# Kernel optimization log

Hardware: AMD Instinct MI355X
Metric: run time of the kernel (lower is better)

The kernel has to match this reference:

```python
import jax, jax.numpy as jnp
import numpy as np
from functools import partial

HID = 320
RF = 4
EPS = 1e-5


def lstm_scan(x_seq, Wih, Whh, bih, bhh):
    """PyTorch-style single-layer LSTM. x_seq: [T,B,D] -> outputs [T,B,H]."""
    T, B, _ = x_seq.shape
    H = Whh.shape[1]
    b = bih + bhh  # [4H]
    # precompute input projections for all steps: [T,B,4H]
    xg = jnp.einsum('tbd,gd->tbg', x_seq, Wih) + b

    def step(carry, xg_t):
        h, c = carry
        gates = xg_t + h @ Whh.T  # [B,4H]
        i, f, g, o = jnp.split(gates, 4, axis=-1)  # torch gate order i,f,g,o
        i = jax.nn.sigmoid(i)
        f = jax.nn.sigmoid(f)
        g = jnp.tanh(g)
        o = jax.nn.sigmoid(o)
        c = f * c + i * g
        h = o * jnp.tanh(c)
        return (h, c), h

    h0 = jnp.zeros((B, H), x_seq.dtype)
    (_, _), ys = jax.lax.scan(step, (h0, h0), xg)
    return ys


def conv2d(x, w, b):
    y = jax.lax.conv_general_dilated(x, w, (1, 1), 'VALID',
                                     dimension_numbers=('NCHW', 'OIHW', 'NCHW'))
    return y + b[None, :, None, None]


def maxpool2(x):
    return jax.lax.reduce_window(x, -jnp.inf, jax.lax.max,
                                 (1, 1, 2, 2), (1, 1, 2, 2), 'VALID')


def batchnorm(x, g, b):
    # training-mode BN (batch statistics, biased variance) like nn.BatchNorm2d
    m = x.mean((0, 2, 3), keepdims=True)
    v = x.var((0, 2, 3), keepdims=True)
    return (x - m) * jax.lax.rsqrt(v + EPS) * g[None, :, None, None] + b[None, :, None, None]


def setup_inputs() -> dict:
    key = jax.random.key(0)
    ks = iter(jax.random.split(key, 64))
    s = 0.05
    d = {}
    d['X'] = jax.random.normal(next(ks), (512, 3, 32, 32), jnp.float32)
    d['conv1_w'] = jax.random.normal(next(ks), (128, 3, 3, 3)) * s
    d['conv1_b'] = jnp.zeros((128,))
    d['bn1_g'] = jnp.ones((128,))
    d['bn1_b'] = jnp.zeros((128,))
    d['conv2_w'] = jax.random.normal(next(ks), (48, 128, 4, 4)) * s
    d['conv2_b'] = jnp.zeros((48,))
    d['bn2_g'] = jnp.ones((48,))
    d['bn2_b'] = jnp.zeros((48,))
    for i, din in zip((1, 2, 3, 4), (48, 48, 640, 640)):
        d[f'rnn{i}_Wih'] = jax.random.normal(next(ks), (4 * HID, din)) * s
        d[f'rnn{i}_Whh'] = jax.random.normal(next(ks), (4 * HID, HID)) * s
        d[f'rnn{i}_bih'] = jnp.zeros((4 * HID,))
        d[f'rnn{i}_bhh'] = jnp.zeros((4 * HID,))
    d['dense1_w'] = jax.random.normal(next(ks), (2048, 40960)) * 0.01
    d['dense1_b'] = jnp.zeros((2048,))
    d['dense2_w'] = jax.random.normal(next(ks), (2048, 12 * 12 * 48)) * 0.01
    d['dense2_b'] = jnp.zeros((2048,))
    d['fc_w'] = jax.random.normal(next(ks), (10, 4096)) * 0.01
    d['fc_b'] = jnp.zeros((10,))
    return d


def reference(X, conv1_w, conv1_b, bn1_g, bn1_b, conv2_w, conv2_b, bn2_g, bn2_b,
              rnn1_Wih, rnn1_Whh, rnn1_bih, rnn1_bhh,
              rnn2_Wih, rnn2_Whh, rnn2_bih, rnn2_bhh,
              rnn3_Wih, rnn3_Whh, rnn3_bih, rnn3_bhh,
              rnn4_Wih, rnn4_Whh, rnn4_bih, rnn4_bhh,
              dense1_w, dense1_b, dense2_w, dense2_b, fc_w, fc_b):
    B = X.shape[0]
    ph = pw = 32 // RF  # 8
    # --- fused patch extraction: [B,3,32,32] -> [B,ph,pw,48] (channel-major features) ---
    patches = (X.reshape(B, 3, ph, RF, pw, RF)
                .transpose(0, 2, 4, 1, 3, 5)
                .reshape(B, ph, pw, RF * RF * 3))
    # vertical fw sequence: t = i*pw + j, element = patches[:, j, i, :]
    v_fw = jnp.transpose(patches, (2, 1, 0, 3)).reshape(ph * pw, B, RF * RF * 3)
    v_rev = v_fw[::-1]
    out1 = lstm_scan(v_fw, rnn1_Wih, rnn1_Whh, rnn1_bih, rnn1_bhh)   # [64,B,320]
    out2 = lstm_scan(v_rev, rnn2_Wih, rnn2_Whh, rnn2_bih, rnn2_bhh)
    vfm = jnp.concatenate([out1, out2], axis=2)                       # [64,B,640]
    vfm = vfm.transpose(1, 0, 2).reshape(B, pw, ph, 2 * HID)          # (permute(0,2,1,3) in src is a no-op: not assigned)
    # horizontal sequences are row-major flatten of vfm
    h_fw = vfm.reshape(B, ph * pw, 2 * HID).transpose(1, 0, 2)        # [64,B,640]
    h_rev = h_fw[::-1]
    out3 = lstm_scan(h_fw, rnn3_Wih, rnn3_Whh, rnn3_bih, rnn3_bhh)
    out4 = lstm_scan(h_rev, rnn4_Wih, rnn4_Whh, rnn4_bih, rnn4_bhh)
    hfm = jnp.concatenate([out3, out4], axis=2).transpose(1, 0, 2).reshape(B, ph * pw * 2 * HID)
    output1 = jax.nn.relu(hfm @ dense1_w.T + dense1_b)                # [B,2048]
    # --- LeNet branch ---
    o2 = batchnorm(maxpool2(jax.nn.relu(conv2d(X, conv1_w, conv1_b))), bn1_g, bn1_b)
    o2 = batchnorm(jax.nn.relu(conv2d(o2, conv2_w, conv2_b)), bn2_g, bn2_b)
    o2 = o2.reshape(B, 12 * 12 * 48)
    output2 = jax.nn.relu(o2 @ dense2_w.T + dense2_b)                 # dropout = identity (eval)
    out = jnp.concatenate([output1, output2], axis=1)                 # [B,4096]
    logits = out @ fc_w.T + fc_b
    return jax.nn.log_softmax(logits, axis=-1)
```

## Files before the change

### kernel.cpp

```cpp
#include <hip/hip_runtime.h>
#include <hip/hip_bf16.h>
#include <math.h>

typedef __hip_bfloat16 bf16;
typedef short bf16x8 __attribute__((ext_vector_type(8)));
typedef float f32x4 __attribute__((ext_vector_type(4)));

__device__ __forceinline__ float sigf(float x) { return 1.f / (1.f + expf(-x)); }

template<typename T> __device__ __forceinline__ T cvt_out(float v);
template<> __device__ __forceinline__ float cvt_out<float>(float v) { return v; }
template<> __device__ __forceinline__ bf16  cvt_out<bf16>(float v)  { return __float2bfloat16(v); }

__device__ __forceinline__ unsigned short f2bu(float x) {
  bf16 b = __float2bfloat16(x);
  return *reinterpret_cast<unsigned short*>(&b);
}

__device__ __forceinline__ void load_lds16(const void* g, void* l) {
  __builtin_amdgcn_global_load_lds(
      (const __attribute__((address_space(1))) unsigned int*)g,
      (__attribute__((address_space(3))) unsigned int*)l,
      16, 0, 0);
}

__global__ void patch_kernel(const float* __restrict__ X, float* __restrict__ v) {
  int idx = blockIdx.x * 256 + threadIdx.x;
  int k = idx % 48;
  int b = (idx / 48) % 512;
  int t = idx / (48 * 512);
  int c = k >> 4, r = (k >> 2) & 3, s = k & 3;
  int ph = t & 7, pw = t >> 3;
  v[idx] = X[((b * 3 + c) * 32 + ph * 4 + r) * 32 + pw * 4 + s];
}

__global__ __launch_bounds__(256) void cvt_f32_bf16_k(const float* __restrict__ in,
                                                      bf16* __restrict__ out, size_t n4) {
  size_t i = (size_t)blockIdx.x * 256 + threadIdx.x;
  if (i >= n4) return;
  float4 v = ((const float4*)in)[i];
  ushort4 o;
  o.x = f2bu(v.x); o.y = f2bu(v.y); o.z = f2bu(v.z); o.w = f2bu(v.w);
  ((ushort4*)out)[i] = o;
}

template<typename OutT, bool RELU>
__global__ __launch_bounds__(256) void gemm_nt(
    const float* __restrict__ A, const float* __restrict__ W,
    const float* __restrict__ b1, const float* __restrict__ b2,
    OutT* __restrict__ C, int M, int N, int K, int ldc) {
  __shared__ float As[16][68];
  __shared__ float Ws[16][68];
  int tid = threadIdx.x;
  int tx = tid & 15, ty = tid >> 4;
  int m0 = blockIdx.y << 6, n0 = blockIdx.x << 6;
  const float* Ap = A + (size_t)m0 * K;
  const float* Wp = W + (size_t)n0 * K;
  float acc[4][4] = {};
  for (int k0 = 0; k0 < K; k0 += 16) {
#pragma unroll
    for (int i = 0; i < 4; i++) {
      int idx = tid + (i << 8);
      int row = idx >> 4, col = idx & 15;
      As[col][row] = Ap[(size_t)row * K + k0 + col];
      Ws[col][row] = Wp[(size_t)row * K + k0 + col];
    }
    __syncthreads();
#pragma unroll
    for (int kk = 0; kk < 16; kk++) {
      float4 av = *(const float4*)&As[kk][ty << 2];
      float4 wv = *(const float4*)&Ws[kk][tx << 2];
      float a[4] = {av.x, av.y, av.z, av.w};
      float w[4] = {wv.x, wv.y, wv.z, wv.w};
#pragma unroll
      for (int i = 0; i < 4; i++)
#pragma unroll
        for (int j = 0; j < 4; j++) acc[i][j] += a[i] * w[j];
    }
    __syncthreads();
  }
#pragma unroll
  for (int i = 0; i < 4; i++) {
    int m = m0 + (ty << 2) + i;
#pragma unroll
    for (int j = 0; j < 4; j++) {
      int n = n0 + (tx << 2) + j;
      float v = acc[i][j];
      if (b1) v += b1[n];
      if (b2) v += b2[n];
      if (RELU) v = fmaxf(v, 0.f);
      C[(size_t)m * ldc + n] = cvt_out<OutT>(v);
    }
  }
}

template<typename OutT, bool RELU, bool SPLITK>
__global__ __launch_bounds__(256) void gemm_mfma(
    const bf16* __restrict__ A, const bf16* __restrict__ W,
    const float* __restrict__ b1, const float* __restrict__ b2,
    OutT* __restrict__ C, int M, int N, int K, int ldc, int ksplit) {
  __shared__ __align__(16) short As[128 * 32];
  __shared__ __align__(16) short Ws[128 * 32];
  int tid = threadIdx.x;
  int m0 = blockIdx.y << 7, n0 = blockIdx.x << 7;
  int kb = SPLITK ? blockIdx.z * ksplit : 0;
  int ke = SPLITK ? kb + ksplit : K;
  int w = tid >> 6, lane = tid & 63;
  int wm = (w >> 1) << 6, wn = (w & 1) << 6;
  int lm = lane & 15, quad = lane >> 4;
  f32x4 acc[4][4];
  f32x4 z4 = {0.f, 0.f, 0.f, 0.f};
#pragma unroll
  for (int i = 0; i < 4; i++)
#pragma unroll
    for (int j = 0; j < 4; j++) acc[i][j] = z4;

  int srow = tid >> 2;
  int soff = (tid & 3) * 8;
  const bf16* Ab  = A + (size_t)(m0 + srow) * K + kb + soff;
  const bf16* Ab2 = Ab + (size_t)64 * K;
  const bf16* Wb  = W + (size_t)(n0 + srow) * K + kb + soff;
  const bf16* Wb2 = Wb + (size_t)64 * K;
  short* AL  = &As[(size_t)tid * 8];
  short* AL2 = &As[(size_t)(tid + 256) * 8];
  short* WL  = &Ws[(size_t)tid * 8];
  short* WL2 = &Ws[(size_t)(tid + 256) * 8];

  for (int k0 = kb; k0 < ke; k0 += 32) {
    load_lds16(Ab, AL);  load_lds16(Ab2, AL2);
    load_lds16(Wb, WL);  load_lds16(Wb2, WL2);
    Ab += 32; Ab2 += 32; Wb += 32; Wb2 += 32;
    __syncthreads();
    bf16x8 af[4], wf[4];
#pragma unroll
    for (int i = 0; i < 4; i++) af[i] = *(const bf16x8*)&As[(wm + i * 16 + lm) * 32 + quad * 8];
#pragma unroll
    for (int j = 0; j < 4; j++) wf[j] = *(const bf16x8*)&Ws[(wn + j * 16 + lm) * 32 + quad * 8];
#pragma unroll
    for (int i = 0; i < 4; i++)
#pragma unroll
      for (int j = 0; j < 4; j++)
        acc[i][j] = __builtin_amdgcn_mfma_f32_16x16x32_bf16(af[i], wf[j], acc[i][j], 0, 0, 0);
    __syncthreads();
  }

  if (SPLITK) {
    float* P = (float*)C + (size_t)blockIdx.z * M * N;
#pragma unroll
    for (int i = 0; i < 4; i++)
#pragma unroll
      for (int j = 0; j < 4; j++) {
        int col = n0 + wn + j * 16 + lm;
        int rowb = m0 + wm + i * 16 + quad * 4;
#pragma unroll
        for (int r = 0; r < 4; r++)
          P[(size_t)(rowb + r) * N + col] = acc[i][j][r];
      }
  } else {
#pragma unroll
    for (int i = 0; i < 4; i++)
#pragma unroll
      for (int j = 0; j < 4; j++) {
        int col = n0 + wn + j * 16 + lm;
        int rowb = m0 + wm + i * 16 + quad * 4;
        float bias = (b1 ? b1[col] : 0.f) + (b2 ? b2[col] : 0.f);
#pragma unroll
        for (int r = 0; r < 4; r++) {
          float v = acc[i][j][r] + bias;
          if (RELU) v = fmaxf(v, 0.f);
          C[(size_t)(rowb + r) * ldc + col] = cvt_out<OutT>(v);
        }
      }
  }
}

__global__ __launch_bounds__(256) void splitk_reduce(const float* __restrict__ P,
                                                     const float* __restrict__ bias,
                                                     float* __restrict__ out,
                                                     int MN, int N, int ldc, int nz) {
  int i = blockIdx.x * 256 + threadIdx.x;
  if (i >= MN) return;
  int m = i / N, n = i - m * N;
  float s = bias[n];
  for (int z = 0; z < nz; z++) s += P[(size_t)z * MN + i];
  out[(size_t)m * ldc + n] = fmaxf(s, 0.f);
}

__global__ __launch_bounds__(256) void lstm_step_mfma(
    const bf16* __restrict__ xgF, const bf16* __restrict__ xgR,
    const bf16* __restrict__ WhhA, const bf16* __restrict__ WhhB,
    const bf16* __restrict__ hinA_hi, const bf16* __restrict__ hinA_lo,
    bf16* __restrict__ houtA_hi, bf16* __restrict__ houtA_lo, float* __restrict__ cA,
    const bf16* __restrict__ hinB_hi, const bf16* __restrict__ hinB_lo,
    bf16* __restrict__ houtB_hi, bf16* __restrict__ houtB_lo, float* __restrict__ cB,
    bf16* __restrict__ outA, bf16* __restrict__ outB, int ldo) {
  int lst = blockIdx.z;
  const bf16* xg  = lst ? xgR : xgF;
  const bf16* Whh = lst ? WhhB : WhhA;
  const bf16* hhi = lst ? hinB_hi : hinA_hi;
  const bf16* hlo = lst ? hinB_lo : hinA_lo;
  bf16* hohi = lst ? houtB_hi : houtA_hi;
  bf16* holo = lst ? houtB_lo : houtA_lo;
  float* c   = lst ? cB : cA;
  bf16* out  = lst ? outB : outA;
  int j0 = blockIdx.x << 5;
  int r0 = blockIdx.y << 6;

  __shared__ __align__(16) short Ah[64 * 32];
  __shared__ __align__(16) short Al[64 * 32];
  __shared__ __align__(16) short Bs[128 * 32];
  __shared__ float G[64 * 129];

  int tid = threadIdx.x;
  int g = tid >> 6, lane = tid & 63;
  int lm = lane & 15, quad = lane >> 4;
  f32x4 acc[4][2];
  f32x4 z4 = {0.f, 0.f, 0.f, 0.f};
#pragma unroll
  for (int i = 0; i < 4; i++) { acc[i][0] = z4; acc[i][1] = z4; }

  int srow = tid >> 2;
  int soff = (tid & 3) * 8;
  const bf16* Ahb = hhi + (size_t)(r0 + srow) * 320 + soff;
  const bf16* Alb = hlo + (size_t)(r0 + srow) * 320 + soff;
  int br1 = tid >> 2;
  int br2 = br1 + 64;
  int grow1 = (br1 >> 5) * 320 + j0 + (br1 & 31);
  int grow2 = (br2 >> 5) * 320 + j0 + (br2 & 31);
  const bf16* Bb1 = Whh + (size_t)grow1 * 320 + soff;
  const bf16* Bb2 = Whh + (size_t)grow2 * 320 + soff;
  short* AhL = &Ah[(size_t)tid * 8];
  short* AlL = &Al[(size_t)tid * 8];
  short* BL1 = &Bs[(size_t)tid * 8];
  short* BL2 = &Bs[(size_t)(tid + 256) * 8];

  for (int k0 = 0; k0 < 320; k0 += 32) {
    load_lds16(Ahb, AhL); load_lds16(Alb, AlL);
    load_lds16(Bb1, BL1); load_lds16(Bb2, BL2);
    Ahb += 32; Alb += 32; Bb1 += 32; Bb2 += 32;
    __syncthreads();
    bf16x8 ah[4], alv[4], bv[2];
#pragma unroll
    for (int i = 0; i < 4; i++) {
      ah[i]  = *(const bf16x8*)&Ah[(i * 16 + lm) * 32 + quad * 8];
      alv[i] = *(const bf16x8*)&Al[(i * 16 + lm) * 32 + quad * 8];
    }
#pragma unroll
    for (int j = 0; j < 2; j++) bv[j] = *(const bf16x8*)&Bs[(g * 32 + j * 16 + lm) * 32 + quad * 8];
#pragma unroll
    for (int i = 0; i < 4; i++)
#pragma unroll
      for (int j = 0; j < 2; j++) {
        acc[i][j] = __builtin_amdgcn_mfma_f32_16x16x32_bf16(ah[i],  bv[j], acc[i][j], 0, 0, 0);
        acc[i][j] = __builtin_amdgcn_mfma_f32_16x16x32_bf16(alv[i], bv[j], acc[i][j], 0, 0, 0);
      }
    __syncthreads();
  }

#pragma unroll
  for (int i = 0; i < 4; i++)
#pragma unroll
    for (int j = 0; j < 2; j++)
#pragma unroll
      for (int r = 0; r < 4; r++)
        G[(i * 16 + quad * 4 + r) * 129 + g * 32 + j * 16 + lm] = acc[i][j][r];
  __syncthreads();

  int rl = tid >> 2;
  int jb = (tid & 3) * 8;
  int r = r0 + rl;
#pragma unroll
  for (int q = 0; q < 8; q++) {
    int jl = jb + q;
    int jh = j0 + jl;
    float pre[4];
#pragma unroll
    for (int g2 = 0; g2 < 4; g2++)
      pre[g2] = G[rl * 129 + g2 * 32 + jl] +
                __bfloat162float(xg[(size_t)r * 1280 + g2 * 320 + jh]);
    float iv = sigf(pre[0]), fv = sigf(pre[1]), gv = tanhf(pre[2]), ov = sigf(pre[3]);
    size_t sb = (size_t)r * 320 + jh;
    float cn = fv * c[sb] + iv * gv;
    float hn = ov * tanhf(cn);
    c[sb] = cn;
    bf16 hb = __float2bfloat16(hn);
    hohi[sb] = hb;
    holo[sb] = __float2bfloat16(hn - __bfloat162float(hb));
    out[(size_t)r * ldo + jh] = hb;
  }
}

__global__ __launch_bounds__(256) void conv1_pool(
    const float* __restrict__ X, const float* __restrict__ w,
    const float* __restrict__ bias, float* __restrict__ pool) {
  int b = blockIdx.x;
  __shared__ float Xs[3 * 32 * 32];
  __shared__ float Wl[128 * 27];
  __shared__ float Bl[128];
  int tid = threadIdx.x;
  for (int i = tid; i < 3072; i += 256) Xs[i] = X[(size_t)b * 3072 + i];
  for (int i = tid; i < 3456; i += 256) Wl[i] = w[i];
  if (tid < 128) Bl[tid] = bias[tid];
  __syncthreads();
  int oc = tid & 127, half = tid >> 7;
  float wr[27];
#pragma unroll
  for (int q = 0; q < 27; q++) wr[q] = Wl[oc * 27 + q];
  float bv = Bl[oc];
  for (int p = half; p < 225; p += 2) {
    int i = p / 15, j = p % 15;
    float mx = -3.4e38f;
#pragma unroll
    for (int dy = 0; dy < 2; dy++)
#pragma unroll
      for (int dx = 0; dx < 2; dx++) {
        float s = bv;
        int rb = 2 * i + dy, cb = 2 * j + dx;
#pragma unroll
        for (int cc = 0; cc < 3; cc++)
#pragma unroll
          for (int kr = 0; kr < 3; kr++)
#pragma unroll
            for (int kc = 0; kc < 3; kc++)
              s += wr[cc * 9 + kr * 3 + kc] * Xs[cc * 1024 + (rb + kr) * 32 + cb + kc];
        mx = fmaxf(mx, s);
      }
    pool[((size_t)(b * 128 + oc)) * 225 + p] = fmaxf(mx, 0.f);
  }
}

__global__ void bn_stats(const float* __restrict__ x, int C, int per, int B,
                         const float* __restrict__ g, const float* __restrict__ bb,
                         float* __restrict__ a, float* __restrict__ s) {
  int c = blockIdx.x;
  int n = B * per;
  float sum = 0.f, sq = 0.f;
  for (int i = threadIdx.x; i < n; i += 256) {
    int b = i / per, p = i - b * per;
    float v = x[((size_t)b * C + c) * per + p];
    sum += v; sq += v * v;
  }
  __shared__ float S1[256], S2[256];
  S1[threadIdx.x] = sum; S2[threadIdx.x] = sq;
  __syncthreads();
  for (int off = 128; off > 0; off >>= 1) {
    if (threadIdx.x < off) { S1[threadIdx.x] += S1[threadIdx.x + off]; S2[threadIdx.x] += S2[threadIdx.x + off]; }
    __syncthreads();
  }
  if (threadIdx.x == 0) {
    float m = S1[0] / n;
    float var = S2[0] / n - m * m;
    float av = g[c] * rsqrtf(var + 1e-5f);
    a[c] = av; s[c] = bb[c] - m * av;
  }
}

__global__ void bn_apply_bf16(const float* __restrict__ x, bf16* __restrict__ y,
                              const float* __restrict__ a, const float* __restrict__ s,
                              int per, int C, size_t total) {
  size_t i = (size_t)blockIdx.x * 256 + threadIdx.x;
  if (i < total) {
    int ch = (int)((i / per) % C);
    y[i] = __float2bfloat16(a[ch] * x[i] + s[ch]);
  }
}

__global__ __launch_bounds__(192) void conv2_kernel(
    const float* __restrict__ pool, const float* __restrict__ w,
    const float* __restrict__ bias, const float* __restrict__ a1,
    const float* __restrict__ s1, float* __restrict__ out) {
  int rg = blockIdx.x, b = blockIdx.y;
  int r0 = rg * 4;
  __shared__ float L[128 * 7 * 15];
  int tid = threadIdx.x;
#pragma unroll
  for (int i = 0; i < 70; i++) {
    int idx = tid + i * 192;
    int c = idx / 105, rem = idx % 105;
    int r = rem / 15, col = rem % 15;
    L[idx] = pool[((size_t)(b * 128 + c)) * 225 + (r0 + r) * 15 + col] * a1[c] + s1[c];
  }
  __syncthreads();
  int oc = tid % 48, orow = tid / 48;
  float acc[12];
  float bv = bias[oc];
#pragma unroll
  for (int j = 0; j < 12; j++) acc[j] = bv;
  for (int c = 0; c < 128; c++) {
#pragma unroll
    for (int kr = 0; kr < 4; kr++) {
      float v[15];
#pragma unroll
      for (int q = 0; q < 15; q++) v[q] = L[(c * 7 + orow + kr) * 15 + q];
      const float* wp = &w[((size_t)(oc * 128 + c)) * 16 + kr * 4];
#pragma unroll
      for (int kc = 0; kc < 4; kc++) {
        float wv = wp[kc];
#pragma unroll
        for (int j = 0; j < 12; j++) acc[j] += wv * v[j + kc];
      }
    }
  }
  float* op = &out[((size_t)(b * 48 + oc)) * 144 + (r0 + orow) * 12];
#pragma unroll
  for (int j = 0; j < 12; j++) op[j] = fmaxf(acc[j], 0.f);
}

__global__ __launch_bounds__(64) void fc_logsoftmax(
    const float* __restrict__ A, const float* __restrict__ W,
    const float* __restrict__ bias, float* __restrict__ out) {
  int b = blockIdx.x, lane = threadIdx.x;
  float acc[10] = {};
  for (int k = lane; k < 4096; k += 64) {
    float x = A[(size_t)b * 4096 + k];
#pragma unroll
    for (int o = 0; o < 10; o++) acc[o] += x * W[o * 4096 + k];
  }
#pragma unroll
  for (int o = 0; o < 10; o++)
    for (int off = 32; off > 0; off >>= 1) acc[o] += __shfl_down(acc[o], off);
  if (lane == 0) {
    float l[10];
    float m = -3.4e38f;
#pragma unroll
    for (int o = 0; o < 10; o++) { l[o] = acc[o] + bias[o]; m = fmaxf(m, l[o]); }
    float se = 0.f;
#pragma unroll
    for (int o = 0; o < 10; o++) se += expf(l[o] - m);
    float ls = logf(se);
#pragma unroll
    for (int o = 0; o < 10; o++) out[b * 10 + o] = l[o] - m - ls;
  }
}

__global__ void zero_k(float* __restrict__ p, size_t n) {
  size_t i = (size_t)blockIdx.x * 256 + threadIdx.x;
  if (i < n) p[i] = 0.f;
}

extern "C" void kernel_launch(void* const* d_in, const int* in_sizes, int n_in,
                              void* d_out, int out_size, void* d_ws, size_t ws_size,
                              hipStream_t stream) {
  const float* X    = (const float*)d_in[0];
  const float* c1w  = (const float*)d_in[1];
  const float* c1b  = (const float*)d_in[2];
  const float* bn1g = (const float*)d_in[3];
  const float* bn1b = (const float*)d_in[4];
  const float* c2w  = (const float*)d_in[5];
  const float* c2b  = (const float*)d_in[6];
  const float* bn2g = (const float*)d_in[7];
  const float* bn2b = (const float*)d_in[8];
  const float *Wih[4], *Whh[4], *bih[4], *bhh[4];
  for (int i = 0; i < 4; i++) {
    Wih[i] = (const float*)d_in[9 + 4 * i];
    Whh[i] = (const float*)d_in[10 + 4 * i];
    bih[i] = (const float*)d_in[11 + 4 * i];
    bhh[i] = (const float*)d_in[12 + 4 * i];
  }
  const float* d1w = (const float*)d_in[25];
  const float* d1b = (const float*)d_in[26];
  const float* d2w = (const float*)d_in[27];
  const float* d2b = (const float*)d_in[28];
  const float* fcw = (const float*)d_in[29];
  const float* fcb = (const float*)d_in[30];
  float* out = (float*)d_out;

  char* p = (char*)d_ws;
  float* v_fw = (float*)p;  p += (size_t)64 * 512 * 48 * 4;
  char* R = p;              p += (size_t)167772160;
  bf16* xgA = (bf16*)R;
  bf16* xgB = xgA + (size_t)41943040;
  bf16* h_fw = (bf16*)p;    p += (size_t)64 * 512 * 640 * 2;
  bf16* hfm  = (bf16*)p;    p += (size_t)512 * 40960 * 2;
  bf16* wih3b = (bf16*)p;   p += (size_t)1280 * 640 * 2;
  bf16* wih4b = (bf16*)p;   p += (size_t)1280 * 640 * 2;
  bf16* whhb[4];
  for (int i = 0; i < 4; i++) { whhb[i] = (bf16*)p; p += (size_t)1280 * 320 * 2; }
  float* states = (float*)p; p += (size_t)3932160;
  float* P = (float*)p;      p += (size_t)4 * 512 * 2048 * 4;
  float* outcat = (float*)p; p += (size_t)512 * 4096 * 4;
  float* bnp = (float*)p;    p += 2048;
  float* pool   = (float*)R;
  float* c2out  = (float*)(R + 58982400);
  bf16*  c2outb = (bf16*)(R + 58982400 + 14155776);
  bf16*  d2wb   = (bf16*)(R + 58982400 + 14155776 + 7077888);
  bf16*  d1wb   = (bf16*)R;
  float* a1 = bnp, *s1 = bnp + 128, *a2 = bnp + 256, *s2 = bnp + 304;

  float* cA = states;
  float* cB = cA + 163840;
  bf16* hb = (bf16*)(cB + 163840);
  bf16* hA0h = hb;             bf16* hA0l = hb + 163840;
  bf16* hA1h = hb + 327680;    bf16* hA1l = hb + 491520;
  bf16* hB0h = hb + 655360;    bf16* hB0l = hb + 819200;
  bf16* hB1h = hb + 983040;    bf16* hB1l = hb + 1146880;

  patch_kernel<<<6144, 256, 0, stream>>>(X, v_fw);
  for (int i = 0; i < 4; i++)
    cvt_f32_bf16_k<<<400, 256, 0, stream>>>(Whh[i], whhb[i], 102400);
  cvt_f32_bf16_k<<<800, 256, 0, stream>>>(Wih[2], wih3b, 204800);
  cvt_f32_bf16_k<<<800, 256, 0, stream>>>(Wih[3], wih4b, 204800);

  gemm_nt<bf16, false><<<dim3(20, 512), 256, 0, stream>>>(v_fw, Wih[0], bih[0], bhh[0], xgA, 32768, 1280, 48, 1280);
  gemm_nt<bf16, false><<<dim3(20, 512), 256, 0, stream>>>(v_fw, Wih[1], bih[1], bhh[1], xgB, 32768, 1280, 48, 1280);

  zero_k<<<3840, 256, 0, stream>>>(states, (size_t)983040);
  for (int t = 0; t < 64; t++) {
    const bf16* xf = xgA + (size_t)t * 655360;
    const bf16* xr = xgB + (size_t)(63 - t) * 655360;
    bf16* oA = h_fw + (size_t)t * 327680;
    if (t & 1)
      lstm_step_mfma<<<dim3(10, 8, 2), 256, 0, stream>>>(xf, xr, whhb[0], whhb[1],
          hA1h, hA1l, hA0h, hA0l, cA, hB1h, hB1l, hB0h, hB0l, cB, oA, oA + 320, 640);
    else
      lstm_step_mfma<<<dim3(10, 8, 2), 256, 0, stream>>>(xf, xr, whhb[0], whhb[1],
          hA0h, hA0l, hA1h, hA1l, cA, hB0h, hB0l, hB1h, hB1l, cB, oA, oA + 320, 640);
  }

  gemm_mfma<bf16, false, false><<<dim3(10, 256, 1), 256, 0, stream>>>(h_fw, wih3b, bih[2], bhh[2], xgA, 32768, 1280, 640, 1280, 0);
  gemm_mfma<bf16, false, false><<<dim3(10, 256, 1), 256, 0, stream>>>(h_fw, wih4b, bih[3], bhh[3], xgB, 32768, 1280, 640, 1280, 0);

  zero_k<<<3840, 256, 0, stream>>>(states, (size_t)983040);
  for (int t = 0; t < 64; t++) {
    const bf16* xf = xgA + (size_t)t * 655360;
    const bf16* xr = xgB + (size_t)(63 - t) * 655360;
    bf16* oA = hfm + (size_t)t * 640;
    if (t & 1)
      lstm_step_mfma<<<dim3(10, 8, 2), 256, 0, stream>>>(xf, xr, whhb[2], whhb[3],
          hA1h, hA1l, hA0h, hA0l, cA, hB1h, hB1l, hB0h, hB0l, cB, oA, oA + 320, 40960);
    else
      lstm_step_mfma<<<dim3(10, 8, 2), 256, 0, stream>>>(xf, xr, whhb[2], whhb[3],
          hA0h, hA0l, hA1h, hA1l, cA, hB0h, hB0l, hB1h, hB1l, cB, oA, oA + 320, 40960);
  }

  cvt_f32_bf16_k<<<81920, 256, 0, stream>>>(d1w, d1wb, 20971520);
  gemm_mfma<float, false, true><<<dim3(16, 4, 4), 256, 0, stream>>>(hfm, d1wb, nullptr, nullptr, P, 512, 2048, 40960, 2048, 10240);
  splitk_reduce<<<4096, 256, 0, stream>>>(P, d1b, outcat, 1048576, 2048, 4096, 4);

  conv1_pool<<<512, 256, 0, stream>>>(X, c1w, c1b, pool);
  bn_stats<<<128, 256, 0, stream>>>(pool, 128, 225, 512, bn1g, bn1b, a1, s1);
  conv2_kernel<<<dim3(3, 512), 192, 0, stream>>>(pool, c2w, c2b, a1, s1, c2out);
  bn_stats<<<48, 256, 0, stream>>>(c2out, 48, 144, 512, bn2g, bn2b, a2, s2);
  bn_apply_bf16<<<13824, 256, 0, stream>>>(c2out, c2outb, a2, s2, 144, 48, (size_t)3538944);

  cvt_f32_bf16_k<<<13824, 256, 0, stream>>>(d2w, d2wb, 3538944);
  gemm_mfma<float, false, true><<<dim3(16, 4, 4), 256, 0, stream>>>(c2outb, d2wb, nullptr, nullptr, P, 512, 2048, 6912, 2048, 1728);
  splitk_reduce<<<4096, 256, 0, stream>>>(P, d2b, outcat + 2048, 1048576, 2048, 4096, 4);

  fc_logsoftmax<<<512, 64, 0, stream>>>(outcat, fcw, fcb, out);
}
```

Measured before the change: 3.964 ms.

## Fuse LSTM time loop into one persistent cooperative kernel with resident Whh

```diff
diff --git a/kernel.cpp b/kernel.cpp
--- a/kernel.cpp
+++ b/kernel.cpp
@@ -1,6 +1,9 @@
 #include <hip/hip_runtime.h>
 #include <hip/hip_bf16.h>
+#include <hip/hip_cooperative_groups.h>
 #include <math.h>
+
+namespace cg = cooperative_groups;
 
 typedef __hip_bfloat16 bf16;
 typedef short bf16x8 __attribute__((ext_vector_type(8)));
@@ -15,6 +18,10 @@
 __device__ __forceinline__ unsigned short f2bu(float x) {
   bf16 b = __float2bfloat16(x);
   return *reinterpret_cast<unsigned short*>(&b);
+}
+__device__ __forceinline__ float bu2f(unsigned short u) {
+  unsigned int x = ((unsigned int)u) << 16;
+  return __uint_as_float(x);
 }
 
 __device__ __forceinline__ void load_lds16(const void* g, void* l) {
@@ -186,107 +193,145 @@
   out[(size_t)m * ldc + n] = fmaxf(s, 0.f);
 }
 
-__global__ __launch_bounds__(256) void lstm_step_mfma(
-    const bf16* __restrict__ xgF, const bf16* __restrict__ xgR,
-    const bf16* __restrict__ WhhA, const bf16* __restrict__ WhhB,
-    const bf16* __restrict__ hinA_hi, const bf16* __restrict__ hinA_lo,
-    bf16* __restrict__ houtA_hi, bf16* __restrict__ houtA_lo, float* __restrict__ cA,
-    const bf16* __restrict__ hinB_hi, const bf16* __restrict__ hinB_lo,
-    bf16* __restrict__ houtB_hi, bf16* __restrict__ houtB_lo, float* __restrict__ cB,
-    bf16* __restrict__ outA, bf16* __restrict__ outB, int ldo) {
+struct ScanArgs {
+  const bf16 *xgF, *xgR, *WhhA, *WhhB;
+  bf16 *h0hiA, *h0loA, *h1hiA, *h1loA; float* cA;
+  bf16 *h0hiB, *h0loB, *h1hiB, *h1loB; float* cB;
+  bf16 *outA, *outB;
+  int ldo; size_t ostep;
+};
+
+__global__ __launch_bounds__(256, 1) void lstm_scan_mfma(ScanArgs a) {
   int lst = blockIdx.z;
-  const bf16* xg  = lst ? xgR : xgF;
-  const bf16* Whh = lst ? WhhB : WhhA;
-  const bf16* hhi = lst ? hinB_hi : hinA_hi;
-  const bf16* hlo = lst ? hinB_lo : hinA_lo;
-  bf16* hohi = lst ? houtB_hi : houtA_hi;
-  bf16* holo = lst ? houtB_lo : houtA_lo;
-  float* c   = lst ? cB : cA;
-  bf16* out  = lst ? outB : outA;
+  const bf16* Whh = lst ? a.WhhB : a.WhhA;
+  bf16* h0hi = lst ? a.h0hiB : a.h0hiA;
+  bf16* h0lo = lst ? a.h0loB : a.h0loA;
+  bf16* h1hi = lst ? a.h1hiB : a.h1hiA;
+  bf16* h1lo = lst ? a.h1loB : a.h1loA;
+  float* c   = lst ? a.cB : a.cA;
+  bf16* ob   = lst ? a.outB : a.outA;
   int j0 = blockIdx.x << 5;
   int r0 = blockIdx.y << 6;
 
-  __shared__ __align__(16) short Ah[64 * 32];
-  __shared__ __align__(16) short Al[64 * 32];
-  __shared__ __align__(16) short Bs[128 * 32];
+  __shared__ __align__(16) short Bf[40960];
+  __shared__ __align__(16) short Ah[2][2048];
+  __shared__ __align__(16) short Al[2][2048];
   __shared__ float G[64 * 129];
 
   int tid = threadIdx.x;
   int g = tid >> 6, lane = tid & 63;
   int lm = lane & 15, quad = lane >> 4;
-  f32x4 acc[4][2];
-  f32x4 z4 = {0.f, 0.f, 0.f, 0.f};
-#pragma unroll
-  for (int i = 0; i < 4; i++) { acc[i][0] = z4; acc[i][1] = z4; }
+  int l8 = lane << 3;
+
+  for (int idx = tid; idx < 5120; idx += 256) {
+    int ln = idx & 63;
+    int j  = (idx >> 6) & 1;
+    int g2 = (idx >> 7) & 3;
+    int kk = idx >> 9;
+    int grow = g2 * 320 + j0 + (j << 4) + (ln & 15);
+    int k    = (kk << 5) + ((ln >> 4) << 3);
+    *(bf16x8*)&Bf[(size_t)idx * 8] = *(const bf16x8*)&Whh[(size_t)grow * 320 + k];
+  }
 
   int srow = tid >> 2;
   int soff = (tid & 3) * 8;
-  const bf16* Ahb = hhi + (size_t)(r0 + srow) * 320 + soff;
-  const bf16* Alb = hlo + (size_t)(r0 + srow) * 320 + soff;
-  int br1 = tid >> 2;
-  int br2 = br1 + 64;
-  int grow1 = (br1 >> 5) * 320 + j0 + (br1 & 31);
-  int grow2 = (br2 >> 5) * 320 + j0 + (br2 & 31);
-  const bf16* Bb1 = Whh + (size_t)grow1 * 320 + soff;
-  const bf16* Bb2 = Whh + (size_t)grow2 * 320 + soff;
-  short* AhL = &Ah[(size_t)tid * 8];
-  short* AlL = &Al[(size_t)tid * 8];
-  short* BL1 = &Bs[(size_t)tid * 8];
-  short* BL2 = &Bs[(size_t)(tid + 256) * 8];
-
-  for (int k0 = 0; k0 < 320; k0 += 32) {
-    load_lds16(Ahb, AhL); load_lds16(Alb, AlL);
-    load_lds16(Bb1, BL1); load_lds16(Bb2, BL2);
-    Ahb += 32; Alb += 32; Bb1 += 32; Bb2 += 32;
-    __syncthreads();
-    bf16x8 ah[4], alv[4], bv[2];
-#pragma unroll
-    for (int i = 0; i < 4; i++) {
-      ah[i]  = *(const bf16x8*)&Ah[(i * 16 + lm) * 32 + quad * 8];
-      alv[i] = *(const bf16x8*)&Al[(i * 16 + lm) * 32 + quad * 8];
-    }
-#pragma unroll
-    for (int j = 0; j < 2; j++) bv[j] = *(const bf16x8*)&Bs[(g * 32 + j * 16 + lm) * 32 + quad * 8];
+  size_t hbase = (size_t)(r0 + srow) * 320 + soff;
+  short* AhL[2] = { &Ah[0][tid * 8], &Ah[1][tid * 8] };
+  short* AlL[2] = { &Al[0][tid * 8], &Al[1][tid * 8] };
+
+  int jb = (tid & 3) * 8;
+  int r = r0 + srow;
+  size_t sb = (size_t)r * 320 + j0 + jb;
+  size_t obase = (size_t)r * a.ldo + j0 + jb;
+
+  cg::grid_group grid = cg::this_grid();
+  __syncthreads();
+
+  for (int t = 0; t < 64; ++t) {
+    const bf16* hih = (t & 1) ? h1hi : h0hi;
+    const bf16* hil = (t & 1) ? h1lo : h0lo;
+    bf16* hoh = (t & 1) ? h0hi : h1hi;
+    bf16* hol = (t & 1) ? h0lo : h1lo;
+    const bf16* xg_t = lst ? a.xgR + (size_t)(63 - t) * 655360
+                           : a.xgF + (size_t)t * 655360;
+
+    f32x4 acc[4][2];
+    f32x4 z4 = {0.f, 0.f, 0.f, 0.f};
+#pragma unroll
+    for (int i = 0; i < 4; i++) { acc[i][0] = z4; acc[i][1] = z4; }
+
+    load_lds16(hih + hbase, AhL[0]);
+    load_lds16(hil + hbase, AlL[0]);
+    __syncthreads();
+    int cur = 0;
+    for (int kk = 0; kk < 10; ++kk) {
+      if (kk < 9) {
+        load_lds16(hih + hbase + (kk + 1) * 32, AhL[cur ^ 1]);
+        load_lds16(hil + hbase + (kk + 1) * 32, AlL[cur ^ 1]);
+      }
+      bf16x8 ah[4], alv[4], bv[2];
+#pragma unroll
+      for (int i = 0; i < 4; i++) {
+        ah[i]  = *(const bf16x8*)&Ah[cur][(i * 16 + lm) * 32 + quad * 8];
+        alv[i] = *(const bf16x8*)&Al[cur][(i * 16 + lm) * 32 + quad * 8];
+      }
+#pragma unroll
+      for (int j = 0; j < 2; j++)
+        bv[j] = *(const bf16x8*)&Bf[(size_t)((kk * 4 + g) * 2 + j) * 512 + l8];
+#pragma unroll
+      for (int i = 0; i < 4; i++)
+#pragma unroll
+        for (int j = 0; j < 2; j++) {
+          acc[i][j] = __builtin_amdgcn_mfma_f32_16x16x32_bf16(ah[i],  bv[j], acc[i][j], 0, 0, 0);
+          acc[i][j] = __builtin_amdgcn_mfma_f32_16x16x32_bf16(alv[i], bv[j], acc[i][j], 0, 0, 0);
+        }
+      __syncthreads();
+      cur ^= 1;
+    }
+
 #pragma unroll
     for (int i = 0; i < 4; i++)
 #pragma unroll
-      for (int j = 0; j < 2; j++) {
-        acc[i][j] = __builtin_amdgcn_mfma_f32_16x16x32_bf16(ah[i],  bv[j], acc[i][j], 0, 0, 0);
-        acc[i][j] = __builtin_amdgcn_mfma_f32_16x16x32_bf16(alv[i], bv[j], acc[i][j], 0, 0, 0);
-      }
-    __syncthreads();
-  }
-
-#pragma unroll
-  for (int i = 0; i < 4; i++)
-#pragma unroll
-    for (int j = 0; j < 2; j++)
-#pragma unroll
-      for (int r = 0; r < 4; r++)
-        G[(i * 16 + quad * 4 + r) * 129 + g * 32 + j * 16 + lm] = acc[i][j][r];
-  __syncthreads();
-
-  int rl = tid >> 2;
-  int jb = (tid & 3) * 8;
-  int r = r0 + rl;
-#pragma unroll
-  for (int q = 0; q < 8; q++) {
-    int jl = jb + q;
-    int jh = j0 + jl;
-    float pre[4];
-#pragma unroll
-    for (int g2 = 0; g2 < 4; g2++)
-      pre[g2] = G[rl * 129 + g2 * 32 + jl] +
-                __bfloat162float(xg[(size_t)r * 1280 + g2 * 320 + jh]);
-    float iv = sigf(pre[0]), fv = sigf(pre[1]), gv = tanhf(pre[2]), ov = sigf(pre[3]);
-    size_t sb = (size_t)r * 320 + jh;
-    float cn = fv * c[sb] + iv * gv;
-    float hn = ov * tanhf(cn);
-    c[sb] = cn;
-    bf16 hb = __float2bfloat16(hn);
-    hohi[sb] = hb;
-    holo[sb] = __float2bfloat16(hn - __bfloat162float(hb));
-    out[(size_t)r * ldo + jh] = hb;
+      for (int j = 0; j < 2; j++)
+#pragma unroll
+        for (int rr = 0; rr < 4; rr++)
+          G[(i * 16 + quad * 4 + rr) * 129 + g * 32 + (j << 4) + lm] = acc[i][j][rr];
+    __syncthreads();
+
+    float pre[4][8];
+    const bf16* xgrow = xg_t + (size_t)r * 1280 + j0 + jb;
+#pragma unroll
+    for (int g2 = 0; g2 < 4; g2++) {
+      bf16x8 xv = *(const bf16x8*)&xgrow[g2 * 320];
+#pragma unroll
+      for (int q = 0; q < 8; q++)
+        pre[g2][q] = G[srow * 129 + g2 * 32 + jb + q] + bu2f((unsigned short)xv[q]);
+    }
+    float cc[8];
+    *(float4*)&cc[0] = *(const float4*)&c[sb];
+    *(float4*)&cc[4] = *(const float4*)&c[sb + 4];
+    bf16x8 vhi, vlo;
+#pragma unroll
+    for (int q = 0; q < 8; q++) {
+      float iv = sigf(pre[0][q]), fv = sigf(pre[1][q]);
+      float gv = tanhf(pre[2][q]), ov = sigf(pre[3][q]);
+      float cn = fv * cc[q] + iv * gv;
+      float hn = ov * tanhf(cn);
+      cc[q] = cn;
+      unsigned short hu = f2bu(hn);
+      vhi[q] = (short)hu;
+      vlo[q] = (short)f2bu(hn - bu2f(hu));
+    }
+    *(float4*)&c[sb]     = *(float4*)&cc[0];
+    *(float4*)&c[sb + 4] = *(float4*)&cc[4];
+    *(bf16x8*)&hoh[sb] = vhi;
+    *(bf16x8*)&hol[sb] = vlo;
+    *(bf16x8*)&ob[(size_t)t * a.ostep + obase] = vhi;
+
+    if (t < 63) {
+      __threadfence();
+      grid.sync();
+    }
   }
 }
 
@@ -505,32 +550,28 @@
   gemm_nt<bf16, false><<<dim3(20, 512), 256, 0, stream>>>(v_fw, Wih[1], bih[1], bhh[1], xgB, 32768, 1280, 48, 1280);
 
   zero_k<<<3840, 256, 0, stream>>>(states, (size_t)983040);
-  for (int t = 0; t < 64; t++) {
-    const bf16* xf = xgA + (size_t)t * 655360;
-    const bf16* xr = xgB + (size_t)(63 - t) * 655360;
-    bf16* oA = h_fw + (size_t)t * 327680;
-    if (t & 1)
-      lstm_step_mfma<<<dim3(10, 8, 2), 256, 0, stream>>>(xf, xr, whhb[0], whhb[1],
-          hA1h, hA1l, hA0h, hA0l, cA, hB1h, hB1l, hB0h, hB0l, cB, oA, oA + 320, 640);
-    else
-      lstm_step_mfma<<<dim3(10, 8, 2), 256, 0, stream>>>(xf, xr, whhb[0], whhb[1],
-          hA0h, hA0l, hA1h, hA1l, cA, hB0h, hB0l, hB1h, hB1l, cB, oA, oA + 320, 640);
+  {
+    ScanArgs sa;
+    sa.xgF = xgA; sa.xgR = xgB; sa.WhhA = whhb[0]; sa.WhhB = whhb[1];
+    sa.h0hiA = hA0h; sa.h0loA = hA0l; sa.h1hiA = hA1h; sa.h1loA = hA1l; sa.cA = cA;
+    sa.h0hiB = hB0h; sa.h0loB = hB0l; sa.h1hiB = hB1h; sa.h1loB = hB1l; sa.cB = cB;
+    sa.outA = h_fw; sa.outB = h_fw + 320; sa.ldo = 640; sa.ostep = 327680;
+    void* ka[] = { &sa };
+    hipLaunchCooperativeKernel((void*)lstm_scan_mfma, dim3(10, 8, 2), dim3(256, 1, 1), ka, 0, stream);
   }
 
   gemm_mfma<bf16, false, false><<<dim3(10, 256, 1), 256, 0, stream>>>(h_fw, wih3b, bih[2], bhh[2], xgA, 32768, 1280, 640, 1280, 0);
   gemm_mfma<bf16, false, false><<<dim3(10, 256, 1), 256, 0, stream>>>(h_fw, wih4b, bih[3], bhh[3], xgB, 32768, 1280, 640, 1280, 0);
 
   zero_k<<<3840, 256, 0, stream>>>(states, (size_t)983040);
-  for (int t = 0; t < 64; t++) {
-    const bf16* xf = xgA + (size_t)t * 655360;
-    const bf16* xr = xgB + (size_t)(63 - t) * 655360;
-    bf16* oA = hfm + (size_t)t * 640;
-    if (t & 1)
-      lstm_step_mfma<<<dim3(10, 8, 2), 256, 0, stream>>>(xf, xr, whhb[2], whhb[3],
-          hA1h, hA1l, hA0h, hA0l, cA, hB1h, hB1l, hB0h, hB0l, cB, oA, oA + 320, 40960);
-    else
-      lstm_step_mfma<<<dim3(10, 8, 2), 256, 0, stream>>>(xf, xr, whhb[2], whhb[3],
-          hA0h, hA0l, hA1h, hA1l, cA, hB0h, hB0l, hB1h, hB1l, cB, oA, oA + 320, 40960);
+  {
+    ScanArgs sb;
+    sb.xgF = xgA; sb.xgR = xgB; sb.WhhA = whhb[2]; sb.WhhB = whhb[3];
+    sb.h0hiA = hA0h; sb.h0loA = hA0l; sb.h1hiA = hA1h; sb.h1loA = hA1l; sb.cA = cA;
+    sb.h0hiB = hB0h; sb.h0loB = hB0l; sb.h1hiB = hB1h; sb.h1loB = hB1l; sb.cB = cB;
+    sb.outA = hfm; sb.outB = hfm + 320; sb.ldo = 40960; sb.ostep = 640;
+    void* ka[] = { &sb };
+    hipLaunchCooperativeKernel((void*)lstm_scan_mfma, dim3(10, 8, 2), dim3(256, 1, 1), ka, 0, stream);
   }
 
   cvt_f32_bf16_k<<<81920, 256, 0, stream>>>(d1w, d1wb, 20971520);
```

New measurement: 9.048 ms. +128.3%, slower.
